# Kernel optimization log

Measured on AMD Instinct MI355X. Metric: run time of the kernel, lower is better.

Reference implementation:

```python
import jax, jax.numpy as jnp
import numpy as np

B_G = 16        # number of point clouds
N_PER = 32768   # points per cloud (equal -> no padding)
T = B_G * N_PER
CIN = 16
D = 32          # global_dim
H = 4           # num_heads
HD = D // H
L = 2           # layers
EPS_LN = 1e-5
EPS_Z = 1e-6


def setup_inputs() -> dict:
    key = jax.random.key(0)
    ks = jax.random.split(key, 32)
    r = lambda i, shape, s: (jax.random.normal(ks[i], shape, dtype=jnp.float32) * s)
    inp = {
        "x": r(0, (T, CIN), 1.0),
        "pos": r(1, (T, 3), 1.0),
        "batch": (jnp.arange(T, dtype=jnp.int32) // N_PER),
        "w_in": r(2, (CIN, D), CIN ** -0.5),
        "b_in": r(3, (D,), 0.02),
        "w_pos": r(4, (3, D), 3 ** -0.5),
        "b_pos": r(5, (D,), 0.02),
        "wq": r(6, (L, D, D), D ** -0.5),
        "bq": r(7, (L, D), 0.02),
        "wk": r(8, (L, D, D), D ** -0.5),
        "bk": r(9, (L, D), 0.02),
        "wv": r(10, (L, D, D), D ** -0.5),
        "bv": r(11, (L, D), 0.02),
        "wo": r(12, (L, D, D), D ** -0.5),
        "bo": r(13, (L, D), 0.02),
        "g1": jnp.ones((L, D), jnp.float32),
        "be1": jnp.zeros((L, D), jnp.float32),
        "w1": r(14, (L, D, 2 * D), D ** -0.5),
        "bf1": r(15, (L, 2 * D), 0.02),
        "w2": r(16, (L, 2 * D, D), (2 * D) ** -0.5),
        "bf2": r(17, (L, D), 0.02),
        "g2": jnp.ones((L, D), jnp.float32),
        "be2": jnp.zeros((L, D), jnp.float32),
    }
    return inp


def _layernorm(h, g, b):
    mu = jnp.mean(h, axis=-1, keepdims=True)
    var = jnp.mean(jnp.square(h - mu), axis=-1, keepdims=True)
    return (h - mu) * jax.lax.rsqrt(var + EPS_LN) * g + b


def _linear_attn(h, wq, bq, wk, bk, wv, bv, wo, bo):
    B, N, C = h.shape
    def heads(w, b):
        return (h @ w + b).reshape(B, N, H, HD).transpose(0, 2, 1, 3)  # [B,H,N,hd]
    q = jax.nn.elu(heads(wq, bq)) + 1.0   # ELU feature map phi(.)
    k = jax.nn.elu(heads(wk, bk)) + 1.0
    v = heads(wv, bv)
    kv = jnp.einsum("bhnd,bhne->bhde", k, v)            # O(N) KV summary
    ksum = k.sum(axis=2)                                   # [B,H,hd]
    z = 1.0 / (jnp.einsum("bhnd,bhd->bhn", q, ksum) + EPS_Z)
    out = jnp.einsum("bhnd,bhde->bhne", q, kv) * z[..., None]
    out = out.transpose(0, 2, 1, 3).reshape(B, N, C)
    return out @ wo + bo


def reference(x, pos, batch, w_in, b_in, w_pos, b_pos, wq, bq, wk, bk, wv, bv,
              wo, bo, g1, be1, w1, bf1, w2, bf2, g2, be2):
    # to_dense_batch: batch is sorted; compute per-point index within its segment
    counts = jax.ops.segment_sum(jnp.ones((T,), jnp.int32), batch, num_segments=B_G)
    starts = jnp.concatenate([jnp.zeros((1,), jnp.int32), jnp.cumsum(counts)[:-1]])
    idx = jnp.arange(T, dtype=jnp.int32) - starts[batch]
    x_dense = jnp.zeros((B_G, N_PER, CIN), x.dtype).at[batch, idx].set(x)
    pos_dense = jnp.zeros((B_G, N_PER, 3), pos.dtype).at[batch, idx].set(pos)

    h = (x_dense @ w_in + b_in) + (pos_dense @ w_pos + b_pos)  # [B,N,D]
    for l in range(L):
        h = _layernorm(h + _linear_attn(h, wq[l], bq[l], wk[l], bk[l],
                                        wv[l], bv[l], wo[l], bo[l]), g1[l], be1[l])
        ffn = jax.nn.relu(h @ w1[l] + bf1[l]) @ w2[l] + bf2[l]
        h = _layernorm(h + ffn, g2[l], be2[l])
    return h[batch, idx]  # back to [T, D] (h[mask])
```

## Files before the change

kernel.cpp:

```cpp
#include <hip/hip_runtime.h>

#define KVSZ 288
#define EPS_LN 1e-5f
#define EPS_Z  1e-6f
#define BS 512

typedef __attribute__((ext_vector_type(8))) short bf16x8;
typedef __attribute__((ext_vector_type(4))) float f32x4;

#define MFMA(a, b, c) __builtin_amdgcn_mfma_f32_16x16x32_bf16(a, b, c, 0, 0, 0)

#define PWE 0
#define LBASE(l) (1024 + (l) * 8192)
#define PQ 0
#define PO 1024
#define P1 2048
#define P2 4096
#define PK 6144
#define PV 7168

__device__ __forceinline__ unsigned short f2bf(float f) {
  union { float f; unsigned u; } x; x.f = f;
  unsigned r = x.u + 0x7fff + ((x.u >> 16) & 1);
  return (unsigned short)(r >> 16);
}

__device__ __forceinline__ unsigned pkbf(float a, float b) {
#if __has_builtin(__builtin_amdgcn_cvt_pk_bf16_f32)
  typedef __attribute__((ext_vector_type(2))) __bf16 bf16x2_t;
  bf16x2_t v = __builtin_amdgcn_cvt_pk_bf16_f32(a, b);
  return __builtin_bit_cast(unsigned, v);
#else
  return (unsigned)f2bf(a) | ((unsigned)f2bf(b) << 16);
#endif
}

__device__ __forceinline__ float bfu(unsigned short s) {
  union { float f; unsigned u; } x; x.u = ((unsigned)s) << 16; return x.f;
}

__device__ __forceinline__ void lds_fence() { asm volatile("s_waitcnt lgkmcnt(0)" ::: "memory"); }
__device__ __forceinline__ float phi(float x) { return x > 0.f ? x + 1.f : __expf(x); }

__device__ __forceinline__ int perm32(int kp) {
  return ((kp & 4) << 2) | (((kp >> 3) << 2) + (kp & 3));
}

__device__ __forceinline__ bf16x8 bbuild(f32x4 lo, f32x4 hi) {
  union { bf16x8 v; unsigned u[4]; } cv;
  cv.u[0] = pkbf(lo[0], lo[1]); cv.u[1] = pkbf(lo[2], lo[3]);
  cv.u[2] = pkbf(hi[0], hi[1]); cv.u[3] = pkbf(hi[2], hi[3]);
  return cv.v;
}

__device__ __forceinline__ void stage_a32(unsigned short* dst, const float* __restrict__ W,
                                          int N, int gt, int gs) {
  for (int i = gt; i < 32 * N; i += gs) {
    int n = i >> 5, kp = i & 31;
    dst[i] = f2bf(W[perm32(kp) * N + n]);
  }
}
__device__ __forceinline__ void stage_a64(unsigned short* dst, const float* __restrict__ W,
                                          int gt, int gs) {
  for (int i = gt; i < 64 * 32; i += gs) {
    int n = i >> 6, kp = i & 63;
    int kl = ((kp >> 5) << 5) + perm32(kp & 31);
    dst[i] = f2bf(W[kl * 32 + n]);
  }
}

__device__ __forceinline__ void stage_kvm_lds(unsigned short* dst,
                                              const float* __restrict__ kvg, int tid) {
  for (int i = tid; i < 1024; i += BS) {
    int e = i >> 5, kp = i & 31;
    int d = perm32(kp);
    float v = ((d >> 3) == (e >> 3)) ? kvg[(e >> 3) * 64 + (d & 7) * 8 + (e & 7)] : 0.f;
    dst[i] = f2bf(v);
  }
}

__device__ __forceinline__ void ln_t(f32x4& a0, f32x4& a1, float4 g0, float4 g1,
                                     float4 b0, float4 b1) {
  float s = a0[0] + a0[1] + a0[2] + a0[3] + a1[0] + a1[1] + a1[2] + a1[3];
  s += __shfl_xor(s, 16); s += __shfl_xor(s, 32);
  float mu = s * (1.f / 32.f);
  float vv = 0.f;
#pragma unroll
  for (int r = 0; r < 4; r++) {
    a0[r] -= mu; a1[r] -= mu;
    vv += a0[r] * a0[r] + a1[r] * a1[r];
  }
  vv += __shfl_xor(vv, 16); vv += __shfl_xor(vv, 32);
  float rstd = rsqrtf(vv * (1.f / 32.f) + EPS_LN);
  a0[0] = a0[0] * rstd * g0.x + b0.x; a0[1] = a0[1] * rstd * g0.y + b0.y;
  a0[2] = a0[2] * rstd * g0.z + b0.z; a0[3] = a0[3] * rstd * g0.w + b0.w;
  a1[0] = a1[0] * rstd * g1.x + b1.x; a1[1] = a1[1] * rstd * g1.y + b1.y;
  a1[2] = a1[2] * rstd * g1.z + b1.z; a1[3] = a1[3] * rstd * g1.w + b1.w;
}

__device__ __forceinline__ void layer_core_l(
    f32x4 (&hc0)[4], f32x4 (&hc1)[4], const bf16x8 (&hBp)[4],
    const unsigned short* lw, const unsigned short* kvm, const float* kss,
    int quad, int m,
    const float* __restrict__ bq, const float* __restrict__ bo,
    const float* __restrict__ g1, const float* __restrict__ be1,
    const float* __restrict__ bf1, const float* __restrict__ bf2,
    const float* __restrict__ g2, const float* __restrict__ be2) {
  const int k0 = quad * 8, q4 = quad * 4;
  {
    const bf16x8 wqA0 = *(const bf16x8*)(lw + PQ + m * 32 + k0);
    const bf16x8 wqA1 = *(const bf16x8*)(lw + PQ + (16 + m) * 32 + k0);
    const bf16x8 woA0 = *(const bf16x8*)(lw + PO + m * 32 + k0);
    const bf16x8 woA1 = *(const bf16x8*)(lw + PO + (16 + m) * 32 + k0);
    const bf16x8 kvA0 = *(const bf16x8*)(kvm + m * 32 + k0);
    const bf16x8 kvA1 = *(const bf16x8*)(kvm + (16 + m) * 32 + k0);
    const float4 bq0 = *(const float4*)(bq + q4), bq1 = *(const float4*)(bq + 16 + q4);
    const float4 bo0 = *(const float4*)(bo + q4), bo1 = *(const float4*)(bo + 16 + q4);
    const float4 g10 = *(const float4*)(g1 + q4), g11 = *(const float4*)(g1 + 16 + q4);
    const float4 e10 = *(const float4*)(be1 + q4), e11 = *(const float4*)(be1 + 16 + q4);
    const float4 ks0 = *(const float4*)(kss + q4);
    const float4 ks1 = *(const float4*)(kss + 16 + q4);
#pragma unroll
    for (int mt = 0; mt < 4; mt++) {
      f32x4 q0 = {bq0.x, bq0.y, bq0.z, bq0.w};
      f32x4 q1 = {bq1.x, bq1.y, bq1.z, bq1.w};
      q0 = MFMA(wqA0, hBp[mt], q0);
      q1 = MFMA(wqA1, hBp[mt], q1);
#pragma unroll
      for (int r = 0; r < 4; r++) { q0[r] = phi(q0[r]); q1[r] = phi(q1[r]); }
      bf16x8 qB = bbuild(q0, q1);
      f32x4 zz = {0.f, 0.f, 0.f, 0.f};
      f32x4 at0 = MFMA(kvA0, qB, zz);
      f32x4 at1 = MFMA(kvA1, qB, zz);
      float p0 = q0[0] * ks0.x + q0[1] * ks0.y + q0[2] * ks0.z + q0[3] * ks0.w;
      float p1 = q1[0] * ks1.x + q1[1] * ks1.y + q1[2] * ks1.z + q1[3] * ks1.w;
      p0 += __shfl_xor(p0, 16);
      p1 += __shfl_xor(p1, 16);
      float z0 = 1.f / (p0 + EPS_Z), z1 = 1.f / (p1 + EPS_Z);
      bf16x8 aB;
      {
        union { bf16x8 v; unsigned u[4]; } cv;
        cv.u[0] = pkbf(at0[0] * z0, at0[1] * z0); cv.u[1] = pkbf(at0[2] * z0, at0[3] * z0);
        cv.u[2] = pkbf(at1[0] * z1, at1[1] * z1); cv.u[3] = pkbf(at1[2] * z1, at1[3] * z1);
        aB = cv.v;
      }
      f32x4 h0 = hc0[mt], h1 = hc1[mt];
      h0[0] += bo0.x; h0[1] += bo0.y; h0[2] += bo0.z; h0[3] += bo0.w;
      h1[0] += bo1.x; h1[1] += bo1.y; h1[2] += bo1.z; h1[3] += bo1.w;
      h0 = MFMA(woA0, aB, h0);
      h1 = MFMA(woA1, aB, h1);
      ln_t(h0, h1, g10, g11, e10, e11);
      hc0[mt] = h0; hc1[mt] = h1;
    }
  }
  {
    bf16x8 w1A[4]; float4 b1f[4];
#pragma unroll
    for (int nt = 0; nt < 4; nt++) {
      w1A[nt] = *(const bf16x8*)(lw + P1 + (nt * 16 + m) * 32 + k0);
      b1f[nt] = *(const float4*)(bf1 + nt * 16 + q4);
    }
    const bf16x8 w2L0 = *(const bf16x8*)(lw + P2 + m * 64 + k0);
    const bf16x8 w2H0 = *(const bf16x8*)(lw + P2 + m * 64 + 32 + k0);
    const bf16x8 w2L1 = *(const bf16x8*)(lw + P2 + (16 + m) * 64 + k0);
    const bf16x8 w2H1 = *(const bf16x8*)(lw + P2 + (16 + m) * 64 + 32 + k0);
    const float4 b20 = *(const float4*)(bf2 + q4), b21 = *(const float4*)(bf2 + 16 + q4);
    const float4 g20 = *(const float4*)(g2 + q4), g21 = *(const float4*)(g2 + 16 + q4);
    const float4 e20 = *(const float4*)(be2 + q4), e21 = *(const float4*)(be2 + 16 + q4);
#pragma unroll
    for (int mt = 0; mt < 4; mt++) {
      bf16x8 hB = bbuild(hc0[mt], hc1[mt]);
      f32x4 hd[4];
#pragma unroll
      for (int nt = 0; nt < 4; nt++) {
        f32x4 ini = {b1f[nt].x, b1f[nt].y, b1f[nt].z, b1f[nt].w};
        hd[nt] = MFMA(w1A[nt], hB, ini);
#pragma unroll
        for (int r = 0; r < 4; r++) hd[nt][r] = fmaxf(hd[nt][r], 0.f);
      }
      bf16x8 fL = bbuild(hd[0], hd[1]);
      bf16x8 fH = bbuild(hd[2], hd[3]);
      f32x4 o0 = hc0[mt], o1 = hc1[mt];
      o0[0] += b20.x; o0[1] += b20.y; o0[2] += b20.z; o0[3] += b20.w;
      o1[0] += b21.x; o1[1] += b21.y; o1[2] += b21.z; o1[3] += b21.w;
      o0 = MFMA(w2L0, fL, o0);
      o0 = MFMA(w2H0, fH, o0);
      o1 = MFMA(w2L1, fL, o1);
      o1 = MFMA(w2H1, fH, o1);
      ln_t(o0, o1, g20, g21, e20, e21);
      hc0[mt] = o0; hc1[mt] = o1;
    }
  }
}

__device__ __forceinline__ void kv_stage_l(
    const bf16x8 (&hBp)[4], unsigned short* tw,
    const unsigned short* lwK, const unsigned short* lwV,
    float* blk, int quad, int m,
    const float* __restrict__ bk, const float* __restrict__ bv) {
  const int k0 = quad * 8, q4 = quad * 4;
  unsigned short* Tk = tw;
  unsigned short* Tv = tw + 1280;
  const bf16x8 wkA0 = *(const bf16x8*)(lwK + m * 32 + k0);
  const bf16x8 wkA1 = *(const bf16x8*)(lwK + (16 + m) * 32 + k0);
  const bf16x8 wvA0 = *(const bf16x8*)(lwV + m * 32 + k0);
  const bf16x8 wvA1 = *(const bf16x8*)(lwV + (16 + m) * 32 + k0);
  const float4 bk0 = *(const float4*)(bk + q4), bk1 = *(const float4*)(bk + 16 + q4);
  const float4 bv0 = *(const float4*)(bv + q4), bv1 = *(const float4*)(bv + 16 + q4);
  f32x4 accA = {0.f, 0.f, 0.f, 0.f}, accB = {0.f, 0.f, 0.f, 0.f};
  f32x4 ksa0 = {0.f, 0.f, 0.f, 0.f}, ksa1 = {0.f, 0.f, 0.f, 0.f};
#pragma unroll
  for (int ch = 0; ch < 2; ch++) {
#pragma unroll
    for (int mtl = 0; mtl < 2; mtl++) {
      int mt = ch * 2 + mtl;
      f32x4 kn0 = {bk0.x, bk0.y, bk0.z, bk0.w};
      f32x4 kn1 = {bk1.x, bk1.y, bk1.z, bk1.w};
      f32x4 vn0 = {bv0.x, bv0.y, bv0.z, bv0.w};
      f32x4 vn1 = {bv1.x, bv1.y, bv1.z, bv1.w};
      kn0 = MFMA(wkA0, hBp[mt], kn0);
      kn1 = MFMA(wkA1, hBp[mt], kn1);
      vn0 = MFMA(wvA0, hBp[mt], vn0);
      vn1 = MFMA(wvA1, hBp[mt], vn1);
      int cb = mtl * 16 + m;
#pragma unroll
      for (int r = 0; r < 4; r++) {
        kn0[r] = phi(kn0[r]); kn1[r] = phi(kn1[r]);
        ksa0[r] += kn0[r];    ksa1[r] += kn1[r];
        Tk[(q4 + r) * 40 + cb]      = f2bf(kn0[r]);
        Tk[(16 + q4 + r) * 40 + cb] = f2bf(kn1[r]);
        Tv[(q4 + r) * 40 + cb]      = f2bf(vn0[r]);
        Tv[(16 + q4 + r) * 40 + cb] = f2bf(vn1[r]);
      }
    }
    lds_fence();
    bf16x8 akL = *(const bf16x8*)(Tk + m * 40 + k0);
    bf16x8 akH = *(const bf16x8*)(Tk + (16 + m) * 40 + k0);
    bf16x8 avL = *(const bf16x8*)(Tv + m * 40 + k0);
    bf16x8 avH = *(const bf16x8*)(Tv + (16 + m) * 40 + k0);
    accA = MFMA(akL, avL, accA);
    accB = MFMA(akH, avH, accB);
    lds_fence();
  }
#pragma unroll
  for (int r = 0; r < 4; r++) {
    float v0 = ksa0[r], v1 = ksa1[r];
    v0 += __shfl_xor(v0, 1); v0 += __shfl_xor(v0, 2); v0 += __shfl_xor(v0, 4); v0 += __shfl_xor(v0, 8);
    v1 += __shfl_xor(v1, 1); v1 += __shfl_xor(v1, 2); v1 += __shfl_xor(v1, 4); v1 += __shfl_xor(v1, 8);
    if (m == 0) {
      atomicAdd(&blk[256 + q4 + r], v0);
      atomicAdd(&blk[272 + q4 + r], v1);
    }
  }
  if ((quad >> 1) == (m >> 3)) {
    int h0 = quad >> 1, h1 = 2 + (quad >> 1), e = m & 7;
#pragma unroll
    for (int r = 0; r < 4; r++) {
      int d = (q4 + r) & 7;
      atomicAdd(&blk[h0 * 64 + d * 8 + e], accA[r]);
      atomicAdd(&blk[h1 * 64 + d * 8 + e], accB[r]);
    }
  }
}

__global__ __launch_bounds__(256) void k_prep(
    const float* __restrict__ w_in, const float* __restrict__ w_pos,
    const float* __restrict__ wq, const float* __restrict__ wk,
    const float* __restrict__ wv, const float* __restrict__ wo,
    const float* __restrict__ w1, const float* __restrict__ w2,
    unsigned short* __restrict__ pw, float* __restrict__ kvbuf) {
  const int gt = blockIdx.x * 256 + threadIdx.x;
  const int gs = gridDim.x * 256;
  for (int i = gt; i < 2 * 16 * KVSZ; i += gs) kvbuf[i] = 0.f;
  for (int i = gt; i < 1024; i += gs) {
    int n = i >> 5, k = i & 31;
    float v = k < 16 ? w_in[k * 32 + n] : (k < 19 ? w_pos[(k - 16) * 32 + n] : 0.f);
    pw[PWE + i] = f2bf(v);
  }
  for (int l = 0; l < 2; l++) {
    unsigned short* b = pw + LBASE(l);
    stage_a32(b + PQ, wq + l * 1024, 32, gt, gs);
    stage_a32(b + PO, wo + l * 1024, 32, gt, gs);
    stage_a32(b + P1, w1 + l * 2048, 64, gt, gs);
    stage_a64(b + P2, w2 + l * 2048, gt, gs);
    stage_a32(b + PK, wk + l * 1024, 32, gt, gs);
    stage_a32(b + PV, wv + l * 1024, 32, gt, gs);
  }
}

template <int H16>
__global__ __launch_bounds__(BS) void k_embed(
    const float* __restrict__ x, const float* __restrict__ pos,
    const float* __restrict__ b_in, const float* __restrict__ b_pos,
    const float* __restrict__ bk, const float* __restrict__ bv,
    const unsigned short* __restrict__ pw, unsigned short* __restrict__ hb,
    float* __restrict__ hf, float* __restrict__ gkv) {
  __shared__ __align__(16) unsigned short lws[3072];
  __shared__ __align__(16) unsigned short tiles[(BS / 64) * 2560];
  __shared__ float blk[KVSZ];
  const int tid = threadIdx.x;
  const int wv_ = tid >> 6, lane = tid & 63, quad = lane >> 4, m = lane & 15;
  unsigned short* tw = tiles + wv_ * 2560;
  const int cloud = blockIdx.x >> 6;
  const int wbase = blockIdx.x * BS + wv_ * 64;
  const int k0 = quad * 8, q4 = quad * 4;
  float4 xt0[4], xt1[4];
  float pp0[4], pp1[4], pp2[4];
#pragma unroll
  for (int mt = 0; mt < 4; mt++) {
    int p = wbase + mt * 16 + m;
    if (quad < 2) {
      const float4* xp = (const float4*)(x + (size_t)p * 16 + quad * 8);
      xt0[mt] = xp[0]; xt1[mt] = xp[1];
    } else if (quad == 2) {
      const float* pq = pos + (size_t)p * 3;
      pp0[mt] = pq[0]; pp1[mt] = pq[1]; pp2[mt] = pq[2];
    }
  }
  for (int j = tid; j < 384; j += BS) {
    int i = j * 8;
    const unsigned short* src = (i < 1024) ? (pw + PWE + i)
                                           : (pw + LBASE(0) + PK + (i - 1024));
    *(bf16x8*)(lws + i) = *(const bf16x8*)src;
  }
  for (int i = tid; i < KVSZ; i += BS) blk[i] = 0.f;
  __syncthreads();
  const bf16x8 weA0 = *(const bf16x8*)(lws + m * 32 + k0);
  const bf16x8 weA1 = *(const bf16x8*)(lws + (16 + m) * 32 + k0);
  float4 bi0, bi1;
  {
    float4 a = *(const float4*)(b_in + q4), b = *(const float4*)(b_pos + q4);
    bi0 = make_float4(a.x + b.x, a.y + b.y, a.z + b.z, a.w + b.w);
    float4 c = *(const float4*)(b_in + 16 + q4), d = *(const float4*)(b_pos + 16 + q4);
    bi1 = make_float4(c.x + d.x, c.y + d.y, c.z + d.z, c.w + d.w);
  }
  bf16x8 fr[4];
#pragma unroll
  for (int mt = 0; mt < 4; mt++) {
    int p = wbase + mt * 16 + m;
    union { bf16x8 v; unsigned u[4]; } xb;
    xb.u[0] = xb.u[1] = xb.u[2] = xb.u[3] = 0;
    if (quad < 2) {
      xb.u[0] = pkbf(xt0[mt].x, xt0[mt].y); xb.u[1] = pkbf(xt0[mt].z, xt0[mt].w);
      xb.u[2] = pkbf(xt1[mt].x, xt1[mt].y); xb.u[3] = pkbf(xt1[mt].z, xt1[mt].w);
    } else if (quad == 2) {
      xb.u[0] = pkbf(pp0[mt], pp1[mt]); xb.u[1] = pkbf(pp2[mt], 0.f);
    }
    f32x4 i0 = {bi0.x, bi0.y, bi0.z, bi0.w};
    f32x4 i1 = {bi1.x, bi1.y, bi1.z, bi1.w};
    f32x4 h0 = MFMA(weA0, xb.v, i0);
    f32x4 h1 = MFMA(weA1, xb.v, i1);
    fr[mt] = bbuild(h0, h1);
    if (H16) {
      *(bf16x8*)(hb + ((size_t)p * 32 + quad * 8)) = fr[mt];
    } else {
      float* hp = hf + (size_t)p * 32;
      *(float4*)(hp + q4)      = make_float4(h0[0], h0[1], h0[2], h0[3]);
      *(float4*)(hp + 16 + q4) = make_float4(h1[0], h1[1], h1[2], h1[3]);
    }
  }
  kv_stage_l(fr, tw, lws + 1024, lws + 2048, blk, quad, m, bk, bv);
  __syncthreads();
  float* g = gkv + cloud * KVSZ;
  for (int i = tid; i < KVSZ; i += BS) atomicAdd(&g[i], blk[i]);
}

template <int H16>
__global__ __launch_bounds__(BS) void k_mid(
    const float* __restrict__ bq, const float* __restrict__ bo,
    const float* __restrict__ g1, const float* __restrict__ be1,
    const float* __restrict__ bf1, const float* __restrict__ bf2,
    const float* __restrict__ g2, const float* __restrict__ be2,
    const float* __restrict__ bkn, const float* __restrict__ bvn,
    const unsigned short* __restrict__ pw, const float* __restrict__ kv_in,
    float* __restrict__ gkv_out, unsigned short* __restrict__ hb,
    float* __restrict__ hf) {
  __shared__ __align__(16) unsigned short lws[8192];
  __shared__ __align__(16) unsigned short kvm[1024];
  __shared__ __align__(16) float kss[32];
  __shared__ __align__(16) unsigned short tiles[(BS / 64) * 2560];
  __shared__ float blk[KVSZ];
  const int tid = threadIdx.x;
  const int wv_ = tid >> 6, lane = tid & 63, quad = lane >> 4, m = lane & 15;
  unsigned short* tw = tiles + wv_ * 2560;
  const int cloud = blockIdx.x >> 6;
  const int wbase = blockIdx.x * BS + wv_ * 64;
  const int q4 = quad * 4;
  const float* kvg = kv_in + cloud * KVSZ;
  bf16x8 fr[4];
  if (H16) {
#pragma unroll
    for (int mt = 0; mt < 4; mt++) {
      int p = wbase + mt * 16 + m;
      fr[mt] = *(const bf16x8*)(hb + ((size_t)p * 32 + quad * 8));
    }
  }
  for (int j = tid; j < 1024; j += BS) {
    int i = j * 8;
    const unsigned short* src = (i < 6144) ? (pw + LBASE(0) + i)
                                           : (pw + LBASE(1) + PK + (i - 6144));
    *(bf16x8*)(lws + i) = *(const bf16x8*)src;
  }
  stage_kvm_lds(kvm, kvg, tid);
  if (tid < 32) kss[tid] = kvg[256 + tid];
  for (int i = tid; i < KVSZ; i += BS) blk[i] = 0.f;
  __syncthreads();
  f32x4 hc0[4], hc1[4];
#pragma unroll
  for (int mt = 0; mt < 4; mt++) {
    if (H16) {
#pragma unroll
      for (int r = 0; r < 4; r++) {
        hc0[mt][r] = bfu((unsigned short)fr[mt][r]);
        hc1[mt][r] = bfu((unsigned short)fr[mt][4 + r]);
      }
    } else {
      int p = wbase + mt * 16 + m;
      const float* hp = hf + (size_t)p * 32;
      float4 lo = *(const float4*)(hp + q4);
      float4 hi = *(const float4*)(hp + 16 + q4);
      hc0[mt][0] = lo.x; hc0[mt][1] = lo.y; hc0[mt][2] = lo.z; hc0[mt][3] = lo.w;
      hc1[mt][0] = hi.x; hc1[mt][1] = hi.y; hc1[mt][2] = hi.z; hc1[mt][3] = hi.w;
      fr[mt] = bbuild(hc0[mt], hc1[mt]);
    }
  }
  layer_core_l(hc0, hc1, fr, lws, kvm, kss, quad, m,
               bq, bo, g1, be1, bf1, bf2, g2, be2);
#pragma unroll
  for (int mt = 0; mt < 4; mt++) {
    int p = wbase + mt * 16 + m;
    fr[mt] = bbuild(hc0[mt], hc1[mt]);
    if (H16) {
      *(bf16x8*)(hb + ((size_t)p * 32 + quad * 8)) = fr[mt];
    } else {
      float* hp = hf + (size_t)p * 32;
      *(float4*)(hp + q4)      = make_float4(hc0[mt][0], hc0[mt][1], hc0[mt][2], hc0[mt][3]);
      *(float4*)(hp + 16 + q4) = make_float4(hc1[mt][0], hc1[mt][1], hc1[mt][2], hc1[mt][3]);
    }
  }
  kv_stage_l(fr, tw, lws + 6144, lws + 7168, blk, quad, m, bkn, bvn);
  __syncthreads();
  float* g = gkv_out + cloud * KVSZ;
  for (int i = tid; i < KVSZ; i += BS) atomicAdd(&g[i], blk[i]);
}

template <int H16>
__global__ __launch_bounds__(BS) void k_last(
    const float* __restrict__ bq, const float* __restrict__ bo,
    const float* __restrict__ g1, const float* __restrict__ be1,
    const float* __restrict__ bf1, const float* __restrict__ bf2,
    const float* __restrict__ g2, const float* __restrict__ be2,
    const unsigned short* __restrict__ pw, const float* __restrict__ kv_in,
    const unsigned short* __restrict__ hb, float* __restrict__ out) {
  __shared__ __align__(16) unsigned short lws[6144];
  __shared__ __align__(16) unsigned short kvm[1024];
  __shared__ __align__(16) float kss[32];
  const int tid = threadIdx.x;
  const int wv_ = tid >> 6, lane = tid & 63, quad = lane >> 4, m = lane & 15;
  const int cloud = blockIdx.x >> 6;
  const int wbase = blockIdx.x * BS + wv_ * 64;
  const int q4 = quad * 4;
  const float* kvg = kv_in + cloud * KVSZ;
  bf16x8 fr[4];
  if (H16) {
#pragma unroll
    for (int mt = 0; mt < 4; mt++) {
      int p = wbase + mt * 16 + m;
      fr[mt] = *(const bf16x8*)(hb + ((size_t)p * 32 + quad * 8));
    }
  }
  for (int j = tid; j < 768; j += BS)
    *(bf16x8*)(lws + j * 8) = *(const bf16x8*)(pw + LBASE(1) + j * 8);
  stage_kvm_lds(kvm, kvg, tid);
  if (tid < 32) kss[tid] = kvg[256 + tid];
  __syncthreads();
  f32x4 hc0[4], hc1[4];
#pragma unroll
  for (int mt = 0; mt < 4; mt++) {
    if (H16) {
#pragma unroll
      for (int r = 0; r < 4; r++) {
        hc0[mt][r] = bfu((unsigned short)fr[mt][r]);
        hc1[mt][r] = bfu((unsigned short)fr[mt][4 + r]);
      }
    } else {
      int p = wbase + mt * 16 + m;
      const float* hp = out + (size_t)p * 32;
      float4 lo = *(const float4*)(hp + q4);
      float4 hi = *(const float4*)(hp + 16 + q4);
      hc0[mt][0] = lo.x; hc0[mt][1] = lo.y; hc0[mt][2] = lo.z; hc0[mt][3] = lo.w;
      hc1[mt][0] = hi.x; hc1[mt][1] = hi.y; hc1[mt][2] = hi.z; hc1[mt][3] = hi.w;
      fr[mt] = bbuild(hc0[mt], hc1[mt]);
    }
  }
  layer_core_l(hc0, hc1, fr, lws, kvm, kss, quad, m,
               bq, bo, g1, be1, bf1, bf2, g2, be2);
#pragma unroll
  for (int mt = 0; mt < 4; mt++) {
    int p = wbase + mt * 16 + m;
    float* hp = out + (size_t)p * 32;
    *(float4*)(hp + q4)      = make_float4(hc0[mt][0], hc0[mt][1], hc0[mt][2], hc0[mt][3]);
    *(float4*)(hp + 16 + q4) = make_float4(hc1[mt][0], hc1[mt][1], hc1[mt][2], hc1[mt][3]);
  }
}

extern "C" void kernel_launch(void* const* d_in, const int* in_sizes, int n_in,
                              void* d_out, int out_size, void* d_ws, size_t ws_size,
                              hipStream_t stream) {
  (void)in_sizes; (void)n_in; (void)out_size;
  const float* x     = (const float*)d_in[0];
  const float* pos   = (const float*)d_in[1];
  const float* w_in  = (const float*)d_in[3];
  const float* b_in  = (const float*)d_in[4];
  const float* w_pos = (const float*)d_in[5];
  const float* b_pos = (const float*)d_in[6];
  const float* wq  = (const float*)d_in[7];
  const float* bq  = (const float*)d_in[8];
  const float* wk  = (const float*)d_in[9];
  const float* bk  = (const float*)d_in[10];
  const float* wv  = (const float*)d_in[11];
  const float* bv  = (const float*)d_in[12];
  const float* wo  = (const float*)d_in[13];
  const float* bo  = (const float*)d_in[14];
  const float* g1  = (const float*)d_in[15];
  const float* be1 = (const float*)d_in[16];
  const float* w1  = (const float*)d_in[17];
  const float* bf1 = (const float*)d_in[18];
  const float* w2  = (const float*)d_in[19];
  const float* bf2 = (const float*)d_in[20];
  const float* g2  = (const float*)d_in[21];
  const float* be2 = (const float*)d_in[22];
  float* out = (float*)d_out;
  float* kvbuf = (float*)d_ws;
  unsigned short* pw = (unsigned short*)((char*)d_ws + 40960);
  unsigned short* hb = (unsigned short*)((char*)d_ws + 131072);
  const size_t need = 131072ull + 524288ull * 32ull * 2ull;
  const bool h16 = ws_size >= need;

  k_prep<<<dim3(64), dim3(256), 0, stream>>>(w_in, w_pos, wq, wk, wv, wo, w1, w2,
                                             pw, kvbuf);
  dim3 grid(524288 / BS), block(BS);
  if (h16) {
    k_embed<1><<<grid, block, 0, stream>>>(x, pos, b_in, b_pos, bk, bv, pw, hb, out, kvbuf);
    k_mid<1><<<grid, block, 0, stream>>>(bq, bo, g1, be1, bf1, bf2, g2, be2,
                                         bk + 32, bv + 32, pw, kvbuf,
                                         kvbuf + 16 * KVSZ, hb, out);
    k_last<1><<<grid, block, 0, stream>>>(bq + 32, bo + 32, g1 + 32, be1 + 32,
                                          bf1 + 64, bf2 + 32, g2 + 32, be2 + 32,
                                          pw, kvbuf + 16 * KVSZ, hb, out);
  } else {
    k_embed<0><<<grid, block, 0, stream>>>(x, pos, b_in, b_pos, bk, bv, pw, hb, out, kvbuf);
    k_mid<0><<<grid, block, 0, stream>>>(bq, bo, g1, be1, bf1, bf2, g2, be2,
                                         bk + 32, bv + 32, pw, kvbuf,
                                         kvbuf + 16 * KVSZ, hb, out);
    k_last<0><<<grid, block, 0, stream>>>(bq + 32, bo + 32, g1 + 32, be1 + 32,
                                          bf1 + 64, bf2 + 32, g2 + 32, be2 + 32,
                                          pw, kvbuf + 16 * KVSZ, hb, out);
  }
}
```

Baseline: 252.4 us.

## Halve block size, swizzle block-to-cloud mapping, pack bf16 conversions

Reduces the block size from 512 to 256 threads with 2048 blocks. It remaps block IDs so consecutive hardware block IDs spread across the 8 XCD-style groups while each cloud's blocks stay contiguous in the logical index. It also converts K/V pairs with a packed bf16 conversion instead of separate scalar rounding. Smaller blocks may raise occupancy and the swizzle balances cloud ownership across dies, at the cost of twice as many per-block weight stagings and global atomic flushes of the KV partials.

```diff
diff --git a/kernel.cpp b/kernel.cpp
--- a/kernel.cpp
+++ b/kernel.cpp
@@ -3,7 +3,8 @@
 #define KVSZ 288
 #define EPS_LN 1e-5f
 #define EPS_Z  1e-6f
-#define BS 512
+#define BS 256
+#define NB 2048
 
 typedef __attribute__((ext_vector_type(8))) short bf16x8;
 typedef __attribute__((ext_vector_type(4))) float f32x4;
@@ -41,6 +42,10 @@
 
 __device__ __forceinline__ void lds_fence() { asm volatile("s_waitcnt lgkmcnt(0)" ::: "memory"); }
 __device__ __forceinline__ float phi(float x) { return x > 0.f ? x + 1.f : __expf(x); }
+
+__device__ __forceinline__ int swz_bid() {
+  return (blockIdx.x & 7) * (NB >> 3) + (blockIdx.x >> 3);
+}
 
 __device__ __forceinline__ int perm32(int kp) {
   return ((kp & 4) << 2) | (((kp >> 3) << 2) + (kp & 3));
@@ -227,10 +232,12 @@
       for (int r = 0; r < 4; r++) {
         kn0[r] = phi(kn0[r]); kn1[r] = phi(kn1[r]);
         ksa0[r] += kn0[r];    ksa1[r] += kn1[r];
-        Tk[(q4 + r) * 40 + cb]      = f2bf(kn0[r]);
-        Tk[(16 + q4 + r) * 40 + cb] = f2bf(kn1[r]);
-        Tv[(q4 + r) * 40 + cb]      = f2bf(vn0[r]);
-        Tv[(16 + q4 + r) * 40 + cb] = f2bf(vn1[r]);
+        unsigned kk = pkbf(kn0[r], kn1[r]);
+        unsigned vv = pkbf(vn0[r], vn1[r]);
+        Tk[(q4 + r) * 40 + cb]      = (unsigned short)kk;
+        Tk[(16 + q4 + r) * 40 + cb] = (unsigned short)(kk >> 16);
+        Tv[(q4 + r) * 40 + cb]      = (unsigned short)vv;
+        Tv[(16 + q4 + r) * 40 + cb] = (unsigned short)(vv >> 16);
       }
     }
     lds_fence();
@@ -301,8 +308,9 @@
   const int tid = threadIdx.x;
   const int wv_ = tid >> 6, lane = tid & 63, quad = lane >> 4, m = lane & 15;
   unsigned short* tw = tiles + wv_ * 2560;
-  const int cloud = blockIdx.x >> 6;
-  const int wbase = blockIdx.x * BS + wv_ * 64;
+  const int bid = swz_bid();
+  const int cloud = bid >> 7;
+  const int wbase = bid * BS + wv_ * 64;
   const int k0 = quad * 8, q4 = quad * 4;
   float4 xt0[4], xt1[4];
   float pp0[4], pp1[4], pp2[4];
@@ -383,8 +391,9 @@
   const int tid = threadIdx.x;
   const int wv_ = tid >> 6, lane = tid & 63, quad = lane >> 4, m = lane & 15;
   unsigned short* tw = tiles + wv_ * 2560;
-  const int cloud = blockIdx.x >> 6;
-  const int wbase = blockIdx.x * BS + wv_ * 64;
+  const int bid = swz_bid();
+  const int cloud = bid >> 7;
+  const int wbase = bid * BS + wv_ * 64;
   const int q4 = quad * 4;
   const float* kvg = kv_in + cloud * KVSZ;
   bf16x8 fr[4];
@@ -457,8 +466,9 @@
   __shared__ __align__(16) float kss[32];
   const int tid = threadIdx.x;
   const int wv_ = tid >> 6, lane = tid & 63, quad = lane >> 4, m = lane & 15;
-  const int cloud = blockIdx.x >> 6;
-  const int wbase = blockIdx.x * BS + wv_ * 64;
+  const int bid = swz_bid();
+  const int cloud = bid >> 7;
+  const int wbase = bid * BS + wv_ * 64;
   const int q4 = quad * 4;
   const float* kvg = kv_in + cloud * KVSZ;
   bf16x8 fr[4];
@@ -539,7 +549,7 @@
 
   k_prep<<<dim3(64), dim3(256), 0, stream>>>(w_in, w_pos, wq, wk, wv, wo, w1, w2,
                                              pw, kvbuf);
-  dim3 grid(524288 / BS), block(BS);
+  dim3 grid(NB), block(BS);
   if (h16) {
     k_embed<1><<<grid, block, 0, stream>>>(x, pos, b_in, b_pos, bk, bv, pw, hb, out, kvbuf);
     k_mid<1><<<grid, block, 0, stream>>>(bq, bo, g1, be1, bf1, bf2, g2, be2,
```

Result: faster. 247.2 us (-2.0%).
